# Kernel tuning notes

Measured on AMD Instinct MI355X. Metric: run time of the kernel, lower is better.

The kernel has to match this reference:

```python
import jax, jax.numpy as jnp
import numpy as np

THRESHOLD = 1.5
MIN_AREA = 3
B, H, W = 8, 1024, 1024


def _label_components(mask):
    """8-connectivity connected-component labeling by min-index propagation.
    mask: [B,H,W] bool. Returns int32 labels [B,H,W]; each component is labeled
    by the minimum global flat index of its pixels; background pixels = B*H*W.
    Labels are globally unique across the batch (matches sort_labels' per-batch
    unique relabeling up to a label permutation).
    """
    N = B * H * W
    SENT = jnp.int32(N)
    flat = jnp.arange(N, dtype=jnp.int32).reshape(B, H, W)
    lab0 = jnp.where(mask, flat, SENT)

    def neighbor_min(lab):
        p = jnp.pad(lab, ((0, 0), (1, 1), (1, 1)), constant_values=N)
        m = lab
        for dr in (-1, 0, 1):
            for dc in (-1, 0, 1):
                if dr == 0 and dc == 0:
                    continue
                m = jnp.minimum(m, p[:, 1 + dr:1 + dr + H, 1 + dc:1 + dc + W])
        return jnp.where(mask, m, SENT)

    def cond(state):
        return state[1]

    def body(state):
        lab, _ = state
        new = neighbor_min(lab)
        return new, jnp.any(new != lab)

    lab, _ = jax.lax.while_loop(cond, body, (lab0, jnp.array(True)))
    return lab


def setup_inputs() -> dict:
    key = jax.random.key(0)
    x = jax.random.normal(key, (B, H, W // 1), dtype=jnp.float32)
    return {"input_tensor": x.reshape(B, 1, H, W)}


def reference(input_tensor):
    """Dense encoding of the original ragged output: for every pixel belonging
    to a cluster with area > MIN_AREA, emit the cluster's max value and the
    (row, col) of the first (lowest flat index) occurrence of that max;
    background / small-cluster pixels get (0, -1, -1). Since THRESHOLD > 0,
    max over masked_fill(0) in the original equals max over cluster pixels.
    """
    x = input_tensor[:, 0]                  # [B,H,W]
    N = B * H * W
    nseg = N + 1                            # last segment = background
    mask = (x >= THRESHOLD)
    ids = _label_components(mask).reshape(-1)          # [N] int32 in [0, N]
    vals = x.reshape(-1)
    fg = mask.reshape(-1)

    area = jax.ops.segment_sum(fg.astype(jnp.float32), ids, num_segments=nseg)
    cmax = jax.ops.segment_max(vals, ids, num_segments=nseg)

    within = jnp.tile(jnp.arange(H * W, dtype=jnp.int32), B)  # flat idx in image
    is_max = (vals == cmax[ids]) & fg
    cand = jnp.where(is_max, within, jnp.int32(H * W))
    amin = jax.ops.segment_min(cand, ids, num_segments=nseg)  # first argmax

    valid = fg & (area[ids] > MIN_AREA)
    out_max = jnp.where(valid, cmax[ids], jnp.float32(0.0)).reshape(B, H, W)
    aidx = amin[ids]
    row = jnp.where(valid, aidx // W, jnp.int32(-1)).reshape(B, H, W)
    col = jnp.where(valid, aidx % W, jnp.int32(-1)).reshape(B, H, W)
    return out_max, row, col
```

## Files before the change

### kernel.cpp

```cpp
#include <hip/hip_runtime.h>
#include <stdint.h>

#define THRESH 1.5f
constexpr int NPIX = 8 * 1024 * 1024;
constexpr int HW   = 1024 * 1024;
constexpr int WW   = 1024;
constexpr int NWORD = NPIX / 32;
constexpr int WPR   = WW / 32;

constexpr int BLK     = 256;
constexpr int GRD_PX4 = NPIX / (BLK * 4);
constexpr int GRD_W   = NWORD / BLK;

constexpr int SPB        = 640;
constexpr int BASE_SLOTS = GRD_W * SPB;
constexpr int OVF_SLOTS  = 16384;
constexpr int CAP        = BASE_SLOTS + OVF_SLOTS;

__device__ __forceinline__ int find_root(const int* __restrict__ P, int x) {
    int p = P[x];
    while (p != x && p < NPIX) { x = p; p = P[x]; }
    return x;
}

__device__ __forceinline__ void merge(int* P, int a, int b) {
    int ra = find_root(P, a);
    int rb = find_root(P, b);
    while (ra != rb) {
        if (ra < rb) { int t = ra; ra = rb; rb = t; }
        int old = atomicCAS(&P[ra], ra, rb);
        if (old == ra) break;
        ra = find_root(P, old);
        rb = find_root(P, rb);
    }
}

__global__ void mask_init_k(const float* __restrict__ x, int* __restrict__ parent,
                            unsigned* __restrict__ mask, int* __restrict__ ovf) {
    __shared__ unsigned s_nib[BLK];
    int t  = threadIdx.x;
    int gt = blockIdx.x * BLK + t;
    int i4 = gt * 4;
    float4 v = *(const float4*)(x + i4);
    unsigned nib = (unsigned)(v.x >= THRESH) | ((unsigned)(v.y >= THRESH) << 1) |
                   ((unsigned)(v.z >= THRESH) << 2) | ((unsigned)(v.w >= THRESH) << 3);
    *(int4*)(parent + i4) = make_int4(i4, i4 + 1, i4 + 2, i4 + 3);
    s_nib[t] = nib;
    __syncthreads();
    if ((t & 7) == 0) {
        unsigned w = 0;
        #pragma unroll
        for (int k = 0; k < 8; k++) w |= s_nib[t + k] << (4 * k);
        mask[gt >> 3] = w;
    }
    if (gt == 0) *ovf = 0;
}

__global__ void union_k(const unsigned* __restrict__ mask, int* __restrict__ parent) {
    int w = blockIdx.x * BLK + threadIdx.x;
    unsigned cur = mask[w];
    if (!cur) return;
    int r  = (w >> 5) & (WW - 1);
    int cw = w & (WPR - 1);
    unsigned prev = (cw > 0) ? mask[w - 1] : 0u;
    unsigned above = 0u, abovePrev = 0u, aboveNext = 0u;
    if (r > 0) {
        above     = mask[w - WPR];
        abovePrev = (cw > 0)       ? mask[w - WPR - 1] : 0u;
        aboveNext = (cw < WPR - 1) ? mask[w - WPR + 1] : 0u;
    }
    int base = w << 5;
    unsigned mW  = cur & ((cur   << 1) | (prev      >> 31));
    unsigned mN  = cur & above;
    unsigned mNW = cur & ((above << 1) | (abovePrev >> 31));
    unsigned mNE = cur & ((above >> 1) | ((aboveNext & 1u) << 31));
    while (mW)  { int b = __ffs(mW)  - 1; mW  &= mW  - 1; merge(parent, base + b, base + b - 1); }
    while (mN)  { int b = __ffs(mN)  - 1; mN  &= mN  - 1; merge(parent, base + b, base + b - WW); }
    while (mNW) { int b = __ffs(mNW) - 1; mNW &= mNW - 1; merge(parent, base + b, base + b - WW - 1); }
    while (mNE) { int b = __ffs(mNE) - 1; mNE &= mNE - 1; merge(parent, base + b, base + b - WW + 1); }
}

__global__ void claim_k(const unsigned* __restrict__ mask, int* __restrict__ parent,
                        int* __restrict__ cnt, unsigned long long* __restrict__ best,
                        int* __restrict__ ovf) {
    __shared__ int s_cnt;
    if (threadIdx.x == 0) s_cnt = 0;
    __syncthreads();
    int w = blockIdx.x * BLK + threadIdx.x;
    unsigned cur = mask[w];
    int base = w << 5;
    while (cur) {
        int b = __ffs(cur) - 1; cur &= cur - 1;
        int p = base + b;
        int root = find_root(parent, p);
        if (root == p) {
            int rank = atomicAdd(&s_cnt, 1);
            int slot;
            if (rank < SPB) slot = blockIdx.x * SPB + rank;
            else { int o = atomicAdd(ovf, 1); slot = BASE_SLOTS + (o < OVF_SLOTS ? o : OVF_SLOTS - 1); }
            cnt[slot] = 0; best[slot] = 0ull;
            parent[p] = NPIX + slot;
        } else {
            parent[p] = root;
        }
    }
}

__device__ __forceinline__ int compact_id(const int* __restrict__ P, int p) {
    int e = P[p];
    if (e < NPIX) e = P[e];
    return e - NPIX;
}

__device__ __forceinline__ void stat_one(const int* __restrict__ parent,
                                         int* __restrict__ cnt,
                                         unsigned long long* __restrict__ best,
                                         int p, float v) {
    int cid = compact_id(parent, p);
    if (cid < 0 || cid >= CAP) return;
    atomicAdd(&cnt[cid], 1);
    unsigned within = (unsigned)(p & (HW - 1));
    unsigned long long pk =
        ((unsigned long long)__float_as_uint(v) << 32) |
        (unsigned long long)(~within);
    atomicMax(&best[cid], pk);
}

__global__ void stats_k(const float* __restrict__ x, const unsigned* __restrict__ mask,
                        const int* __restrict__ parent, int* __restrict__ cnt,
                        unsigned long long* __restrict__ best) {
    int t = blockIdx.x * BLK + threadIdx.x;
    unsigned nib = (mask[t >> 3] >> ((t & 7) * 4)) & 0xFu;
    if (!nib) return;
    int i4 = t * 4;
    float4 v = *(const float4*)(x + i4);
    if (nib & 1u) stat_one(parent, cnt, best, i4,     v.x);
    if (nib & 2u) stat_one(parent, cnt, best, i4 + 1, v.y);
    if (nib & 4u) stat_one(parent, cnt, best, i4 + 2, v.z);
    if (nib & 8u) stat_one(parent, cnt, best, i4 + 3, v.w);
}

__device__ __forceinline__ void lookup_one(const int* __restrict__ parent,
                                           const int* __restrict__ cnt,
                                           const unsigned long long* __restrict__ best,
                                           int p, float& om, float& orow, float& ocol) {
    int cid = compact_id(parent, p);
    if (cid >= 0 && cid < CAP && cnt[cid] > 3) {
        unsigned long long pk = best[cid];
        om   = __uint_as_float((unsigned)(pk >> 32));
        unsigned idx = ~((unsigned)pk);
        orow = (float)(idx >> 10);
        ocol = (float)(idx & (WW - 1));
    }
}

__global__ void out_k(const unsigned* __restrict__ mask, const int* __restrict__ parent,
                      const int* __restrict__ cnt,
                      const unsigned long long* __restrict__ best,
                      float* __restrict__ o) {
    int t = blockIdx.x * BLK + threadIdx.x;
    unsigned nib = (mask[t >> 3] >> ((t & 7) * 4)) & 0xFu;
    int i4 = t * 4;
    float4 m  = make_float4(0.f, 0.f, 0.f, 0.f);
    float4 rr = make_float4(-1.f, -1.f, -1.f, -1.f);
    float4 cc = make_float4(-1.f, -1.f, -1.f, -1.f);
    if (nib) {
        if (nib & 1u) lookup_one(parent, cnt, best, i4,     m.x, rr.x, cc.x);
        if (nib & 2u) lookup_one(parent, cnt, best, i4 + 1, m.y, rr.y, cc.y);
        if (nib & 4u) lookup_one(parent, cnt, best, i4 + 2, m.z, rr.z, cc.z);
        if (nib & 8u) lookup_one(parent, cnt, best, i4 + 3, m.w, rr.w, cc.w);
    }
    *(float4*)(o + i4)            = m;
    *(float4*)(o + NPIX + i4)     = rr;
    *(float4*)(o + 2 * NPIX + i4) = cc;
}

extern "C" void kernel_launch(void* const* d_in, const int* in_sizes, int n_in,
                              void* d_out, int out_size, void* d_ws, size_t ws_size,
                              hipStream_t stream) {
    const float* x = (const float*)d_in[0];
    float* o = (float*)d_out;

    char* base = (char*)d_ws;
    int* parent = (int*)base;
    size_t off = (size_t)NPIX * sizeof(int);
    unsigned long long* best = (unsigned long long*)(base + off);
    int* cnt       = (int*)(base + off + (size_t)CAP * 8);
    unsigned* mask = (unsigned*)(base + off + (size_t)CAP * 12);
    int* ovf       = (int*)(base + off + (size_t)CAP * 12 + (size_t)NWORD * 4);

    mask_init_k<<<GRD_PX4, BLK, 0, stream>>>(x, parent, mask, ovf);
    union_k    <<<GRD_W,   BLK, 0, stream>>>(mask, parent);
    claim_k    <<<GRD_W,   BLK, 0, stream>>>(mask, parent, cnt, best, ovf);
    stats_k    <<<GRD_PX4, BLK, 0, stream>>>(x, mask, parent, cnt, best);
    out_k      <<<GRD_PX4, BLK, 0, stream>>>(mask, parent, cnt, best, o);
}
```

Measured before the change: 218.9 us.

## Drop compact-label claim pass and index component stats by union-find root

Removes the claim kernel that assigned compact slot ids to roots. Stats are now stored in full-size cnt/best arrays indexed directly by root pixel. mask_init zeroes these arrays for foreground pixels, and stats_k compresses each pixel's parent to its root so out_k can read parent[p] directly. This saves one launch and a pass over all foreground pixels, at the cost of larger per-pixel cnt/best workspace, more scattered atomics, and a reliance on stats_k's path compression finishing before out_k runs.

```diff
diff --git a/kernel.cpp b/kernel.cpp
--- a/kernel.cpp
+++ b/kernel.cpp
@@ -12,14 +12,9 @@
 constexpr int GRD_PX4 = NPIX / (BLK * 4);
 constexpr int GRD_W   = NWORD / BLK;
 
-constexpr int SPB        = 640;
-constexpr int BASE_SLOTS = GRD_W * SPB;
-constexpr int OVF_SLOTS  = 16384;
-constexpr int CAP        = BASE_SLOTS + OVF_SLOTS;
-
 __device__ __forceinline__ int find_root(const int* __restrict__ P, int x) {
     int p = P[x];
-    while (p != x && p < NPIX) { x = p; p = P[x]; }
+    while (p != x) { x = p; p = P[x]; }
     return x;
 }
 
@@ -36,7 +31,8 @@
 }
 
 __global__ void mask_init_k(const float* __restrict__ x, int* __restrict__ parent,
-                            unsigned* __restrict__ mask, int* __restrict__ ovf) {
+                            unsigned* __restrict__ mask, int* __restrict__ cnt,
+                            unsigned long long* __restrict__ best) {
     __shared__ unsigned s_nib[BLK];
     int t  = threadIdx.x;
     int gt = blockIdx.x * BLK + t;
@@ -45,6 +41,11 @@
     unsigned nib = (unsigned)(v.x >= THRESH) | ((unsigned)(v.y >= THRESH) << 1) |
                    ((unsigned)(v.z >= THRESH) << 2) | ((unsigned)(v.w >= THRESH) << 3);
     *(int4*)(parent + i4) = make_int4(i4, i4 + 1, i4 + 2, i4 + 3);
+    if (nib) {
+        *(int4*)(cnt + i4) = make_int4(0, 0, 0, 0);
+        ((ulonglong2*)(best + i4))[0] = make_ulonglong2(0ull, 0ull);
+        ((ulonglong2*)(best + i4))[1] = make_ulonglong2(0ull, 0ull);
+    }
     s_nib[t] = nib;
     __syncthreads();
     if ((t & 7) == 0) {
@@ -53,7 +54,6 @@
         for (int k = 0; k < 8; k++) w |= s_nib[t + k] << (4 * k);
         mask[gt >> 3] = w;
     }
-    if (gt == 0) *ovf = 0;
 }
 
 __global__ void union_k(const unsigned* __restrict__ mask, int* __restrict__ parent) {
@@ -80,54 +80,22 @@
     while (mNE) { int b = __ffs(mNE) - 1; mNE &= mNE - 1; merge(parent, base + b, base + b - WW + 1); }
 }
 
-__global__ void claim_k(const unsigned* __restrict__ mask, int* __restrict__ parent,
-                        int* __restrict__ cnt, unsigned long long* __restrict__ best,
-                        int* __restrict__ ovf) {
-    __shared__ int s_cnt;
-    if (threadIdx.x == 0) s_cnt = 0;
-    __syncthreads();
-    int w = blockIdx.x * BLK + threadIdx.x;
-    unsigned cur = mask[w];
-    int base = w << 5;
-    while (cur) {
-        int b = __ffs(cur) - 1; cur &= cur - 1;
-        int p = base + b;
-        int root = find_root(parent, p);
-        if (root == p) {
-            int rank = atomicAdd(&s_cnt, 1);
-            int slot;
-            if (rank < SPB) slot = blockIdx.x * SPB + rank;
-            else { int o = atomicAdd(ovf, 1); slot = BASE_SLOTS + (o < OVF_SLOTS ? o : OVF_SLOTS - 1); }
-            cnt[slot] = 0; best[slot] = 0ull;
-            parent[p] = NPIX + slot;
-        } else {
-            parent[p] = root;
-        }
-    }
-}
-
-__device__ __forceinline__ int compact_id(const int* __restrict__ P, int p) {
-    int e = P[p];
-    if (e < NPIX) e = P[e];
-    return e - NPIX;
-}
-
-__device__ __forceinline__ void stat_one(const int* __restrict__ parent,
+__device__ __forceinline__ void stat_one(int* __restrict__ parent,
                                          int* __restrict__ cnt,
                                          unsigned long long* __restrict__ best,
                                          int p, float v) {
-    int cid = compact_id(parent, p);
-    if (cid < 0 || cid >= CAP) return;
-    atomicAdd(&cnt[cid], 1);
+    int r = find_root(parent, p);
+    if (r != p) parent[p] = r;
+    atomicAdd(&cnt[r], 1);
     unsigned within = (unsigned)(p & (HW - 1));
     unsigned long long pk =
         ((unsigned long long)__float_as_uint(v) << 32) |
         (unsigned long long)(~within);
-    atomicMax(&best[cid], pk);
+    atomicMax(&best[r], pk);
 }
 
 __global__ void stats_k(const float* __restrict__ x, const unsigned* __restrict__ mask,
-                        const int* __restrict__ parent, int* __restrict__ cnt,
+                        int* __restrict__ parent, int* __restrict__ cnt,
                         unsigned long long* __restrict__ best) {
     int t = blockIdx.x * BLK + threadIdx.x;
     unsigned nib = (mask[t >> 3] >> ((t & 7) * 4)) & 0xFu;
@@ -144,9 +112,9 @@
                                            const int* __restrict__ cnt,
                                            const unsigned long long* __restrict__ best,
                                            int p, float& om, float& orow, float& ocol) {
-    int cid = compact_id(parent, p);
-    if (cid >= 0 && cid < CAP && cnt[cid] > 3) {
-        unsigned long long pk = best[cid];
+    int r = parent[p];
+    if (cnt[r] > 3) {
+        unsigned long long pk = best[r];
         om   = __uint_as_float((unsigned)(pk >> 32));
         unsigned idx = ~((unsigned)pk);
         orow = (float)(idx >> 10);
@@ -183,15 +151,12 @@
 
     char* base = (char*)d_ws;
     int* parent = (int*)base;
-    size_t off = (size_t)NPIX * sizeof(int);
-    unsigned long long* best = (unsigned long long*)(base + off);
-    int* cnt       = (int*)(base + off + (size_t)CAP * 8);
-    unsigned* mask = (unsigned*)(base + off + (size_t)CAP * 12);
-    int* ovf       = (int*)(base + off + (size_t)CAP * 12 + (size_t)NWORD * 4);
+    unsigned long long* best = (unsigned long long*)(base + (size_t)NPIX * 4);
+    int* cnt       = (int*)(base + (size_t)NPIX * 12);
+    unsigned* mask = (unsigned*)(base + (size_t)NPIX * 16);
 
-    mask_init_k<<<GRD_PX4, BLK, 0, stream>>>(x, parent, mask, ovf);
+    mask_init_k<<<GRD_PX4, BLK, 0, stream>>>(x, parent, mask, cnt, best);
     union_k    <<<GRD_W,   BLK, 0, stream>>>(mask, parent);
-    claim_k    <<<GRD_W,   BLK, 0, stream>>>(mask, parent, cnt, best, ovf);
     stats_k    <<<GRD_PX4, BLK, 0, stream>>>(x, mask, parent, cnt, best);
     out_k      <<<GRD_PX4, BLK, 0, stream>>>(mask, parent, cnt, best, o);
 }
```

New measurement: 261.6 us. 19.5% more time.

## Compact foreground pixels into per-block worklist for stats kernel

Applied to the files above, without the earlier changes.

During mask initialization, each block appends its foreground pixels (index and value) to a per-block worklist. The stats kernel then launches 64-thread blocks that walk only these compacted entries, instead of scanning every pixel nibble and reloading the input. This targets the sparse foreground (about 6.7% of pixels above the threshold), where most stats threads had no work. The cost is an extra shared atomic and scattered worklist writes in mask_init, a larger workspace, and less coalesced stats work per block.

```diff
diff --git a/kernel.cpp b/kernel.cpp
--- a/kernel.cpp
+++ b/kernel.cpp
@@ -16,6 +16,8 @@
 constexpr int BASE_SLOTS = GRD_W * SPB;
 constexpr int OVF_SLOTS  = 16384;
 constexpr int CAP        = BASE_SLOTS + OVF_SLOTS;
+
+constexpr int WLSTRIDE = 1024;
 
 __device__ __forceinline__ int find_root(const int* __restrict__ P, int x) {
     int p = P[x];
@@ -36,8 +38,10 @@
 }
 
 __global__ void mask_init_k(const float* __restrict__ x, int* __restrict__ parent,
-                            unsigned* __restrict__ mask, int* __restrict__ ovf) {
+                            unsigned* __restrict__ mask, uint2* __restrict__ wl,
+                            int* __restrict__ wl_cnt, int* __restrict__ ovf) {
     __shared__ unsigned s_nib[BLK];
+    __shared__ int s_rank;
     int t  = threadIdx.x;
     int gt = blockIdx.x * BLK + t;
     int i4 = gt * 4;
@@ -45,6 +49,7 @@
     unsigned nib = (unsigned)(v.x >= THRESH) | ((unsigned)(v.y >= THRESH) << 1) |
                    ((unsigned)(v.z >= THRESH) << 2) | ((unsigned)(v.w >= THRESH) << 3);
     *(int4*)(parent + i4) = make_int4(i4, i4 + 1, i4 + 2, i4 + 3);
+    if (t == 0) s_rank = 0;
     s_nib[t] = nib;
     __syncthreads();
     if ((t & 7) == 0) {
@@ -53,6 +58,17 @@
         for (int k = 0; k < 8; k++) w |= s_nib[t + k] << (4 * k);
         mask[gt >> 3] = w;
     }
+    int nfg = __popc(nib);
+    if (nfg) {
+        int r = atomicAdd(&s_rank, nfg);
+        uint2* dst = wl + (size_t)blockIdx.x * WLSTRIDE;
+        if (nib & 1u) dst[r++] = make_uint2((unsigned)i4,     __float_as_uint(v.x));
+        if (nib & 2u) dst[r++] = make_uint2((unsigned)i4 + 1, __float_as_uint(v.y));
+        if (nib & 4u) dst[r++] = make_uint2((unsigned)i4 + 2, __float_as_uint(v.z));
+        if (nib & 8u) dst[r++] = make_uint2((unsigned)i4 + 3, __float_as_uint(v.w));
+    }
+    __syncthreads();
+    if (t == 0) wl_cnt[blockIdx.x] = s_rank;
     if (gt == 0) *ovf = 0;
 }
 
@@ -112,32 +128,23 @@
     return e - NPIX;
 }
 
-__device__ __forceinline__ void stat_one(const int* __restrict__ parent,
-                                         int* __restrict__ cnt,
-                                         unsigned long long* __restrict__ best,
-                                         int p, float v) {
-    int cid = compact_id(parent, p);
-    if (cid < 0 || cid >= CAP) return;
-    atomicAdd(&cnt[cid], 1);
-    unsigned within = (unsigned)(p & (HW - 1));
-    unsigned long long pk =
-        ((unsigned long long)__float_as_uint(v) << 32) |
-        (unsigned long long)(~within);
-    atomicMax(&best[cid], pk);
-}
-
-__global__ void stats_k(const float* __restrict__ x, const unsigned* __restrict__ mask,
+__global__ void stats_k(const uint2* __restrict__ wl, const int* __restrict__ wl_cnt,
                         const int* __restrict__ parent, int* __restrict__ cnt,
                         unsigned long long* __restrict__ best) {
-    int t = blockIdx.x * BLK + threadIdx.x;
-    unsigned nib = (mask[t >> 3] >> ((t & 7) * 4)) & 0xFu;
-    if (!nib) return;
-    int i4 = t * 4;
-    float4 v = *(const float4*)(x + i4);
-    if (nib & 1u) stat_one(parent, cnt, best, i4,     v.x);
-    if (nib & 2u) stat_one(parent, cnt, best, i4 + 1, v.y);
-    if (nib & 4u) stat_one(parent, cnt, best, i4 + 2, v.z);
-    if (nib & 8u) stat_one(parent, cnt, best, i4 + 3, v.w);
+    int region = blockIdx.x;
+    int c = wl_cnt[region];
+    const uint2* src = wl + (size_t)region * WLSTRIDE;
+    for (int j = threadIdx.x; j < c; j += 64) {
+        uint2 e = src[j];
+        int p = (int)e.x;
+        int cid = compact_id(parent, p);
+        if (cid < 0 || cid >= CAP) continue;
+        atomicAdd(&cnt[cid], 1);
+        unsigned within = (unsigned)(p & (HW - 1));
+        unsigned long long pk =
+            ((unsigned long long)e.y << 32) | (unsigned long long)(~within);
+        atomicMax(&best[cid], pk);
+    }
 }
 
 __device__ __forceinline__ void lookup_one(const int* __restrict__ parent,
@@ -183,15 +190,17 @@
 
     char* base = (char*)d_ws;
     int* parent = (int*)base;
-    size_t off = (size_t)NPIX * sizeof(int);
-    unsigned long long* best = (unsigned long long*)(base + off);
-    int* cnt       = (int*)(base + off + (size_t)CAP * 8);
-    unsigned* mask = (unsigned*)(base + off + (size_t)CAP * 12);
-    int* ovf       = (int*)(base + off + (size_t)CAP * 12 + (size_t)NWORD * 4);
-
-    mask_init_k<<<GRD_PX4, BLK, 0, stream>>>(x, parent, mask, ovf);
+    size_t off = (size_t)NPIX * 4;
+    unsigned long long* best = (unsigned long long*)(base + off);  off += (size_t)CAP * 8;
+    int* cnt       = (int*)(base + off);                           off += (size_t)CAP * 4;
+    unsigned* mask = (unsigned*)(base + off);                      off += (size_t)NWORD * 4;
+    int* wl_cnt    = (int*)(base + off);                           off += (size_t)GRD_PX4 * 4;
+    uint2* wl      = (uint2*)(base + off);                         off += (size_t)GRD_PX4 * WLSTRIDE * 8;
+    int* ovf       = (int*)(base + off);
+
+    mask_init_k<<<GRD_PX4, BLK, 0, stream>>>(x, parent, mask, wl, wl_cnt, ovf);
     union_k    <<<GRD_W,   BLK, 0, stream>>>(mask, parent);
     claim_k    <<<GRD_W,   BLK, 0, stream>>>(mask, parent, cnt, best, ovf);
-    stats_k    <<<GRD_PX4, BLK, 0, stream>>>(x, mask, parent, cnt, best);
+    stats_k    <<<GRD_PX4, 64,  0, stream>>>(wl, wl_cnt, parent, cnt, best);
     out_k      <<<GRD_PX4, BLK, 0, stream>>>(mask, parent, cnt, best, o);
 }
```

Result: faster. 202.9 us (-7.3%).
